# Kernel tuning notes

Hardware: AMD Instinct MI355X
Metric: run time of the kernel (lower is better)

The kernel has to match this reference:

```python
import jax, jax.numpy as jnp
import numpy as np
from jax import lax

B, L, C, P = 512, 6, 4, 45

def _conv(x, w, b, pad):
    y = lax.conv_general_dilated(x, w, (1, 1), [(pad, pad), (pad, pad)],
                                 dimension_numbers=('NCHW', 'OIHW', 'NCHW'))
    return y + b[None, :, None, None]

def _maxpool2(x):
    return lax.reduce_window(x, -jnp.inf, lax.max, (1, 1, 2, 2), (1, 1, 2, 2), 'VALID')

def _prelu(x, a):
    return jnp.where(x >= 0, x, a * x)

def setup_inputs() -> dict:
    key = jax.random.key(0)
    ks = jax.random.split(key, 16)
    s = 0.05
    inp = {
        'x': jax.random.normal(ks[0], (B, L, C, P, P), jnp.float32),
        'w0': jax.random.normal(ks[1], (32, C, 5, 5), jnp.float32) * s,
        'b0': jnp.zeros((32,), jnp.float32),
        'w1': jax.random.normal(ks[2], (32, 32, 5, 5), jnp.float32) * s,
        'b1': jnp.zeros((32,), jnp.float32),
        'w2': jax.random.normal(ks[3], (64, 32, 4, 4), jnp.float32) * s,
        'b2': jnp.zeros((64,), jnp.float32),
        'w3': jax.random.normal(ks[4], (64, 64, 3, 3), jnp.float32) * s,
        'b3': jnp.zeros((64,), jnp.float32),
        'a0': jnp.float32(0.25), 'a1': jnp.float32(0.25),
        'a2': jnp.float32(0.25), 'a3': jnp.float32(0.25),
        'fc1_w': jax.random.normal(ks[5], (L, 256, 128), jnp.float32) * s,
        'fc1_b': jnp.zeros((L, 128), jnp.float32),
        'a4': jnp.full((L, 1), 0.25, jnp.float32),
        'fc2_w': jax.random.normal(ks[6], (L, 128, 64), jnp.float32) * s,
        'fc2_b': jnp.zeros((L, 64), jnp.float32),
        'a5': jnp.full((L, 1), 0.25, jnp.float32),
        'fc3_w': jax.random.normal(ks[7], (L, 64, 4), jnp.float32) * s,
        'fc3_b': jnp.zeros((L, 4), jnp.float32),
    }
    return inp

def reference(x, w0, b0, w1, b1, w2, b2, w3, b3, a0, a1, a2, a3,
              fc1_w, fc1_b, a4, fc2_w, fc2_b, a5, fc3_w, fc3_b):
    b, l = x.shape[0], x.shape[1]
    # Conv tower shares weights across landmarks -> fold landmark into batch.
    h = x.reshape(b * l, x.shape[2], P, P)
    h = _maxpool2(_prelu(_conv(h, w0, b0, 1), a0))   # (BL,32,21,21)
    h = _maxpool2(_prelu(_conv(h, w1, b1, 1), a1))   # (BL,32,9,9)
    h = _maxpool2(_prelu(_conv(h, w2, b2, 1), a2))   # (BL,64,4,4)
    h = _prelu(_conv(h, w3, b3, 0), a3)              # (BL,64,2,2)
    h = h.reshape(b, l, 256)
    # Per-landmark FC heads as batched GEMMs.
    h = _prelu(jnp.einsum('bli,lio->blo', h, fc1_w) + fc1_b, a4)
    h = _prelu(jnp.einsum('bli,lio->blo', h, fc2_w) + fc2_b, a5)
    out = jnp.einsum('bli,lio->blo', h, fc3_w) + fc3_b   # (B,L,4)
    return out
```

## Files before the change

### kernel.cpp

```cpp
#include <hip/hip_runtime.h>
#include <stdint.h>

typedef _Float16 f16;
typedef _Float16 half8 __attribute__((ext_vector_type(8)));
typedef _Float16 half4 __attribute__((ext_vector_type(4)));
typedef float floatx16 __attribute__((ext_vector_type(16)));

#define NIMG 3072

#define WS_W0T   0
#define WS_W1T   10240
#define WS_W2T   61440
#define WS_W3T   126976
#define WS_FC1T  200704
#define WS_FC2T  593920
#define WS_FC3T  692224
#define WS_H3F   720896

#define Z16 {0.f,0.f,0.f,0.f,0.f,0.f,0.f,0.f,0.f,0.f,0.f,0.f,0.f,0.f,0.f,0.f}

__global__ __launch_bounds__(256) void k_prep(
    const float* __restrict__ w0, const float* __restrict__ w1, const float* __restrict__ w2,
    const float* __restrict__ w3, const float* __restrict__ fc1w, const float* __restrict__ fc2w,
    const float* __restrict__ fc3w,
    f16* __restrict__ w0t, f16* __restrict__ w1t, f16* __restrict__ w2t, f16* __restrict__ w3t,
    f16* __restrict__ fc1t, f16* __restrict__ fc2t, f16* __restrict__ fc3t)
{
  int stride = gridDim.x * blockDim.x;
  int g0 = blockIdx.x * blockDim.x + threadIdx.x;
  for (int i = g0; i < 5120; i += stride) {
    int j = i & 7, co = (i >> 3) & 31, hf = (i >> 8) & 1, ch = (i >> 9) & 1, ky = i >> 10;
    int k = ch * 16 + hf * 8 + j;
    f16 v = (f16)0.f;
    if (k < 20) { int kx = k >> 2, ci = k & 3; v = (f16)w0[((co * 4 + ci) * 5 + ky) * 5 + kx]; }
    w0t[i] = v;
  }
  for (int i = g0; i < 25600; i += stride) {
    int j = i & 7, co = (i >> 3) & 31, hf = (i >> 8) & 1, ch = (i >> 9) & 1, tap = i >> 10;
    int ci = ch * 16 + hf * 8 + j, ky = tap / 5, kx = tap % 5;
    w1t[i] = (f16)w1[((co * 32 + ci) * 5 + ky) * 5 + kx];
  }
  for (int i = g0; i < 32768; i += stride) {
    int j = i & 7, co = (i >> 3) & 31, hf = (i >> 8) & 1, ct = (i >> 9) & 1, ch = (i >> 10) & 1, tap = i >> 11;
    int ci = ch * 16 + hf * 8 + j, cog = ct * 32 + co, ky = tap >> 2, kx = tap & 3;
    w2t[i] = (f16)w2[((cog * 32 + ci) * 4 + ky) * 4 + kx];
  }
  for (int i = g0; i < 36864; i += stride) {
    int j = i & 7, col = (i >> 3) & 31, hf = (i >> 8) & 1, ct = (i >> 9) & 1, c = i >> 10;
    int k = c * 16 + hf * 8 + j, tap = k >> 6, ci = k & 63, co = ct * 32 + col;
    int ky = tap / 3, kx = tap % 3;
    w3t[i] = (f16)w3[((co * 64 + ci) * 3 + ky) * 3 + kx];
  }
  for (int i = g0; i < 196608; i += stride) {
    int j = i & 7, col = (i >> 3) & 31, hf = (i >> 8) & 1, nt = (i >> 9) & 3, c = (i >> 11) & 15, l = i >> 15;
    int k = c * 16 + hf * 8 + j, o = nt * 32 + col;
    fc1t[i] = (f16)fc1w[(l * 256 + k) * 128 + o];
  }
  for (int i = g0; i < 49152; i += stride) {
    int j = i & 7, col = (i >> 3) & 31, hf = (i >> 8) & 1, nt = (i >> 9) & 1, c = (i >> 10) & 7, l = i >> 13;
    int k = c * 16 + hf * 8 + j, o = nt * 32 + col;
    fc2t[i] = (f16)fc2w[(l * 128 + k) * 64 + o];
  }
  for (int i = g0; i < 12288; i += stride) {
    int j = i & 7, col = (i >> 3) & 31, hf = (i >> 8) & 1, c = (i >> 9) & 3, l = i >> 11;
    int k = c * 16 + hf * 8 + j;
    f16 v = (f16)0.f;
    if (col < 4) v = (f16)fc3w[(l * 64 + k) * 4 + col];
    fc3t[i] = v;
  }
}

__global__ __launch_bounds__(512) void k_conv012(
    const float* __restrict__ x,
    const f16* __restrict__ w0t, const float* __restrict__ b0, const float* __restrict__ a0p,
    const f16* __restrict__ w1t, const float* __restrict__ b1, const float* __restrict__ a1p,
    const f16* __restrict__ w2t, const float* __restrict__ b2, const float* __restrict__ a2p,
    f16* __restrict__ h3f)
{
  __shared__ __align__(16) uint32_t smem_u[16704];
  f16* sh   = (f16*)smem_u;
  f16* s_x  = sh;
  f16* s_h1 = sh + 10528;
  f16* s_h2 = sh;

  const int n = blockIdx.x, tid = threadIdx.x;
  const int wv = tid >> 6, l = tid & 63;
  const int hf = l >> 5, m = l & 31, dr = m >> 3, dc = m & 7, col = m;
  const float a0 = a0p[0], a1 = a1p[0];
  const float b0c = b0[col], b1c = b1[col];
  const half8* w0t8 = (const half8*)w0t;
  const half8* w1t8 = (const half8*)w1t;
  const half8* w2t8 = (const half8*)w2t;

  for (int i = tid; i < 16704; i += 512) smem_u[i] = 0u;
  __syncthreads();
  const float* xin = x + n * 8100;
  for (int i = tid; i < 8100; i += 512) {
    int ci = i / 2025, r = i % 2025;
    int y = r / 45, xx = r % 45;
    s_x[((y + 1) * 56 + (xx + 1)) * 4 + ci] = (f16)xin[i];
  }
  __syncthreads();

  half8 B0[5][2];
  #pragma unroll
  for (int ky = 0; ky < 5; ++ky)
    #pragma unroll
    for (int ch = 0; ch < 2; ++ch)
      B0[ky][ch] = w0t8[(ky * 2 + ch) * 64 + hf * 32 + col];

  const int r0lut0[11] = {0,4,8,12,16,20,24,28,32,36,38};
  for (int t = wv; t < 66; t += 8) {
    int r0 = r0lut0[t / 6], cb = (t % 6) * 8;
    int rowb = r0 + dr, colb = cb + dc;
    const f16* pA = s_x + (rowb * 56 + colb + 2 * hf) * 4;
    floatx16 acc = Z16;
    #pragma unroll
    for (int ky = 0; ky < 5; ++ky) {
      const f16* p = pA + ky * 224;
      half4 l0  = *(const half4*)(p);
      half4 h0  = *(const half4*)(p + 4);
      half4 l1  = *(const half4*)(p + 16);
      half4 h1v = *(const half4*)(p + 20);
      half8 a0v = __builtin_shufflevector(l0, h0, 0,1,2,3,4,5,6,7);
      half8 a1v = __builtin_shufflevector(l1, h1v, 0,1,2,3,4,5,6,7);
      acc = __builtin_amdgcn_mfma_f32_32x32x16_f16(a0v, B0[ky][0], acc, 0, 0, 0);
      acc = __builtin_amdgcn_mfma_f32_32x32x16_f16(a1v, B0[ky][1], acc, 0, 0, 0);
    }
    #pragma unroll
    for (int pp = 0; pp < 2; ++pp)
      #pragma unroll
      for (int c2 = 0; c2 < 2; ++c2) {
        float v = fmaxf(fmaxf(acc[8*pp + 2*c2], acc[8*pp + 2*c2 + 1]),
                        fmaxf(acc[8*pp + 4 + 2*c2], acc[8*pp + 4 + 2*c2 + 1]));
        v += b0c; v = (v >= 0.f) ? v : a0 * v;
        int pr = (r0 >> 1) + pp, pc = (cb >> 1) + 2 * hf + c2;
        if (pc < 21) s_h1[((pr + 1) * 26 + (pc + 1)) * 40 + col] = (f16)v;
      }
  }
  __syncthreads();

  for (int i = tid; i < 2880; i += 512) smem_u[i] = 0u;
  __syncthreads();

  const int r0lut1[5] = {0, 4, 8, 12, 14};
  const int cclut[3]  = {0, 8, 14};
  int t0 = wv * 2;
  int t1 = t0 + 1; if (t1 > 14) t1 = 14;
  int r0a = r0lut1[t0 / 3], cca = cclut[t0 % 3];
  int r0b = r0lut1[t1 / 3], ccb = cclut[t1 % 3];
  const f16* pAa = s_h1 + ((r0a + dr) * 26 + cca + dc) * 40 + hf * 8;
  const f16* pAb = s_h1 + ((r0b + dr) * 26 + ccb + dc) * 40 + hf * 8;
  floatx16 accA = Z16;
  floatx16 accB = Z16;
  for (int ky = 0; ky < 5; ++ky) {
    const half8* wb = w1t8 + ky * 640 + hf * 32 + col;
    const f16* qa = pAa + ky * 1040;
    const f16* qb = pAb + ky * 1040;
    #pragma unroll
    for (int kx = 0; kx < 5; ++kx) {
      #pragma unroll
      for (int ch = 0; ch < 2; ++ch) {
        half8 b  = wb[kx * 128 + ch * 64];
        half8 aA = *(const half8*)(qa + kx * 40 + ch * 16);
        half8 aB = *(const half8*)(qb + kx * 40 + ch * 16);
        accA = __builtin_amdgcn_mfma_f32_32x32x16_f16(aA, b, accA, 0, 0, 0);
        accB = __builtin_amdgcn_mfma_f32_32x32x16_f16(aB, b, accB, 0, 0, 0);
      }
    }
  }
  #pragma unroll
  for (int tt = 0; tt < 2; ++tt) {
    const floatx16 acc = tt ? accB : accA;
    int r0 = tt ? r0b : r0a, cc = tt ? ccb : cca;
    #pragma unroll
    for (int pp = 0; pp < 2; ++pp)
      #pragma unroll
      for (int c2 = 0; c2 < 2; ++c2) {
        float v = fmaxf(fmaxf(acc[8*pp + 2*c2], acc[8*pp + 2*c2 + 1]),
                        fmaxf(acc[8*pp + 4 + 2*c2], acc[8*pp + 4 + 2*c2 + 1]));
        v += b1c; v = (v >= 0.f) ? v : a1 * v;
        int pr = (r0 >> 1) + pp, pc = (cc >> 1) + 2 * hf + c2;
        if (pc < 9) s_h2[((pr + 1) * 12 + (pc + 1)) * 40 + col] = (f16)v;
      }
  }
  __syncthreads();

  if (wv < 2) {
    const int ct = wv;
    const float a2 = a2p[0];
    const float b2c = b2[ct * 32 + col];
    const f16* pA0 = s_h2 + (dr * 12 + dc) * 40 + hf * 8;
    const f16* pA4 = s_h2 + ((4 + dr) * 12 + dc) * 40 + hf * 8;
    floatx16 acc0 = Z16;
    floatx16 acc4 = Z16;
    for (int tap = 0; tap < 16; ++tap) {
      int ky = tap >> 2, kx = tap & 3;
      int aoff = (ky * 12 + kx) * 40;
      #pragma unroll
      for (int ch = 0; ch < 2; ++ch) {
        half8 b  = w2t8[tap * 256 + ch * 128 + ct * 64 + hf * 32 + col];
        half8 a0v = *(const half8*)(pA0 + aoff + ch * 16);
        half8 a4v = *(const half8*)(pA4 + aoff + ch * 16);
        acc0 = __builtin_amdgcn_mfma_f32_32x32x16_f16(a0v, b, acc0, 0, 0, 0);
        acc4 = __builtin_amdgcn_mfma_f32_32x32x16_f16(a4v, b, acc4, 0, 0, 0);
      }
    }
    f16* o = h3f + n * 1024;
    #pragma unroll
    for (int tt = 0; tt < 2; ++tt) {
      const floatx16 acc = tt ? acc4 : acc0;
      #pragma unroll
      for (int pp = 0; pp < 2; ++pp)
        #pragma unroll
        for (int c2 = 0; c2 < 2; ++c2) {
          float v = fmaxf(fmaxf(acc[8*pp + 2*c2], acc[8*pp + 2*c2 + 1]),
                          fmaxf(acc[8*pp + 4 + 2*c2], acc[8*pp + 4 + 2*c2 + 1]));
          v += b2c; v = (v >= 0.f) ? v : a2 * v;
          int pr = tt * 2 + pp, pc = 2 * hf + c2, co = ct * 32 + col;
          o[(pr * 4 + pc) * 64 + co] = (f16)v;
        }
    }
  }
}

__global__ __launch_bounds__(256) void k_tail(
    const f16* __restrict__ h3f,
    const f16* __restrict__ w3t, const float* __restrict__ b3, const float* __restrict__ a3p,
    const f16* __restrict__ fc1t, const float* __restrict__ fc1b, const float* __restrict__ a4,
    const f16* __restrict__ fc2t, const float* __restrict__ fc2b, const float* __restrict__ a5,
    const f16* __restrict__ fc3t, const float* __restrict__ fc3b,
    float* __restrict__ out)
{
  __shared__ __align__(16) f16 s_feat[32 * 264];
  __shared__ __align__(16) f16 s_g1[32 * 136];
  __shared__ __align__(16) f16 s_g2[32 * 72];

  const int lm = blockIdx.x % 6, t = blockIdx.x / 6;
  const int tid = threadIdx.x, wv = tid >> 6, lane = tid & 63;
  const int hf = lane >> 5, col = lane & 31;
  const half8* w3t8  = (const half8*)w3t;
  const half8* fc1t8 = (const half8*)fc1t;
  const half8* fc2t8 = (const half8*)fc2t;
  const half8* fc3t8 = (const half8*)fc3t;

  {
    const int mt = wv;
    const int i_img = mt * 8 + (col >> 2);
    const int pos = col & 3, oy = pos >> 1, ox = pos & 1;
    const int gimg = (t * 32 + i_img) * 6 + lm;
    const f16* Abase = h3f + gimg * 1024 + (oy * 4 + ox) * 64;
    floatx16 acc0 = Z16, acc1 = Z16;
    for (int c = 0; c < 36; ++c) {
      int tap = c >> 2;
      int ky = tap / 3, kx = tap % 3;
      half8 a = *(const half8*)(Abase + (ky * 4 + kx) * 64 + (c & 3) * 16 + hf * 8);
      half8 bb0 = w3t8[((c * 2 + 0) * 2 + hf) * 32 + col];
      half8 bb1 = w3t8[((c * 2 + 1) * 2 + hf) * 32 + col];
      acc0 = __builtin_amdgcn_mfma_f32_32x32x16_f16(a, bb0, acc0, 0, 0, 0);
      acc1 = __builtin_amdgcn_mfma_f32_32x32x16_f16(a, bb1, acc1, 0, 0, 0);
    }
    const float a3 = a3p[0];
    #pragma unroll
    for (int ct = 0; ct < 2; ++ct) {
      const floatx16 acc = ct ? acc1 : acc0;
      const int co = ct * 32 + col;
      const float bb = b3[co];
      #pragma unroll
      for (int q = 0; q < 4; ++q) {
        int ii = mt * 8 + 2 * q + hf;
        half4 w;
        #pragma unroll
        for (int z = 0; z < 4; ++z) {
          float v = acc[q * 4 + z] + bb;
          v = (v >= 0.f) ? v : a3 * v;
          w[z] = (f16)v;
        }
        *(half4*)(s_feat + ii * 264 + co * 4) = w;
      }
    }
  }
  __syncthreads();

  {
    floatx16 g = Z16;
    for (int c = 0; c < 16; ++c) {
      half8 a = *(const half8*)(s_feat + col * 264 + c * 16 + hf * 8);
      half8 b = fc1t8[(((lm * 16 + c) * 4 + wv) * 2 + hf) * 32 + col];
      g = __builtin_amdgcn_mfma_f32_32x32x16_f16(a, b, g, 0, 0, 0);
    }
    const float a4v = a4[lm];
    const float bb = fc1b[lm * 128 + wv * 32 + col];
    #pragma unroll
    for (int reg = 0; reg < 16; ++reg) {
      int r = (reg & 3) + 8 * (reg >> 2) + 4 * hf;
      float v = g[reg] + bb;
      v = (v >= 0.f) ? v : a4v * v;
      s_g1[r * 136 + wv * 32 + col] = (f16)v;
    }
  }
  __syncthreads();

  if (wv < 2) {
    floatx16 g = Z16;
    for (int c = 0; c < 8; ++c) {
      half8 a = *(const half8*)(s_g1 + col * 136 + c * 16 + hf * 8);
      half8 b = fc2t8[(((lm * 8 + c) * 2 + wv) * 2 + hf) * 32 + col];
      g = __builtin_amdgcn_mfma_f32_32x32x16_f16(a, b, g, 0, 0, 0);
    }
    const float a5v = a5[lm];
    const float bb = fc2b[lm * 64 + wv * 32 + col];
    #pragma unroll
    for (int reg = 0; reg < 16; ++reg) {
      int r = (reg & 3) + 8 * (reg >> 2) + 4 * hf;
      float v = g[reg] + bb;
      v = (v >= 0.f) ? v : a5v * v;
      s_g2[r * 72 + wv * 32 + col] = (f16)v;
    }
  }
  __syncthreads();

  if (wv == 0) {
    floatx16 g = Z16;
    for (int c = 0; c < 4; ++c) {
      half8 a = *(const half8*)(s_g2 + col * 72 + c * 16 + hf * 8);
      half8 b = fc3t8[((lm * 4 + c) * 2 + hf) * 32 + col];
      g = __builtin_amdgcn_mfma_f32_32x32x16_f16(a, b, g, 0, 0, 0);
    }
    if (col < 4) {
      const float bb = fc3b[lm * 4 + col];
      #pragma unroll
      for (int reg = 0; reg < 16; ++reg) {
        int r = (reg & 3) + 8 * (reg >> 2) + 4 * hf;
        out[((t * 32 + r) * 6 + lm) * 4 + col] = g[reg] + bb;
      }
    }
  }
}

extern "C" void kernel_launch(void* const* d_in, const int* in_sizes, int n_in,
                              void* d_out, int out_size, void* d_ws, size_t ws_size,
                              hipStream_t stream) {
  const float* x    = (const float*)d_in[0];
  const float* w0   = (const float*)d_in[1];
  const float* b0   = (const float*)d_in[2];
  const float* w1   = (const float*)d_in[3];
  const float* b1   = (const float*)d_in[4];
  const float* w2   = (const float*)d_in[5];
  const float* b2   = (const float*)d_in[6];
  const float* w3   = (const float*)d_in[7];
  const float* b3   = (const float*)d_in[8];
  const float* a0   = (const float*)d_in[9];
  const float* a1   = (const float*)d_in[10];
  const float* a2   = (const float*)d_in[11];
  const float* a3   = (const float*)d_in[12];
  const float* fc1w = (const float*)d_in[13];
  const float* fc1b = (const float*)d_in[14];
  const float* a4   = (const float*)d_in[15];
  const float* fc2w = (const float*)d_in[16];
  const float* fc2b = (const float*)d_in[17];
  const float* a5   = (const float*)d_in[18];
  const float* fc3w = (const float*)d_in[19];
  const float* fc3b = (const float*)d_in[20];
  float* out = (float*)d_out;

  char* ws = (char*)d_ws;
  f16* w0t  = (f16*)(ws + WS_W0T);
  f16* w1t  = (f16*)(ws + WS_W1T);
  f16* w2t  = (f16*)(ws + WS_W2T);
  f16* w3t  = (f16*)(ws + WS_W3T);
  f16* fc1t = (f16*)(ws + WS_FC1T);
  f16* fc2t = (f16*)(ws + WS_FC2T);
  f16* fc3t = (f16*)(ws + WS_FC3T);
  f16* h3f  = (f16*)(ws + WS_H3F);

  k_prep   <<<128, 256, 0, stream>>>(w0, w1, w2, w3, fc1w, fc2w, fc3w,
                                     w0t, w1t, w2t, w3t, fc1t, fc2t, fc3t);
  k_conv012<<<NIMG, 512, 0, stream>>>(x, w0t, b0, a0, w1t, b1, a1, w2t, b2, a2, h3f);
  k_tail   <<<96, 256, 0, stream>>>(h3f, w3t, b3, a3, fc1t, fc1b, a4,
                                    fc2t, fc2b, a5, fc3t, fc3b, out);
}
```

Before: 338.9 us.

## Fuse conv3 and per-landmark FC heads into the per-image conv kernel

Merges the tail kernel into the per-image conv kernel. Each block now computes conv3 and the three FC layers for its own image using scalar FMA dot products on shared-memory fp32 activations, in place of batched MFMA GEMMs over 32 images. This removes the h3f global round trip and one kernel launch. Each block now reads its landmark's FC weights, about 64K fp16 for fc1, so total weight traffic through L2 grows roughly 32x, and the conv2 stage is spread over four waves instead of two.

```diff
diff --git a/kernel.cpp b/kernel.cpp
--- a/kernel.cpp
+++ b/kernel.cpp
@@ -11,11 +11,10 @@
 #define WS_W0T   0
 #define WS_W1T   10240
 #define WS_W2T   61440
-#define WS_W3T   126976
-#define WS_FC1T  200704
-#define WS_FC2T  593920
-#define WS_FC3T  692224
-#define WS_H3F   720896
+#define WS_W3G   126976
+#define WS_FC1G  200704
+#define WS_FC2G  593920
+#define WS_FC3G  692224
 
 #define Z16 {0.f,0.f,0.f,0.f,0.f,0.f,0.f,0.f,0.f,0.f,0.f,0.f,0.f,0.f,0.f,0.f}
 
@@ -23,8 +22,8 @@
     const float* __restrict__ w0, const float* __restrict__ w1, const float* __restrict__ w2,
     const float* __restrict__ w3, const float* __restrict__ fc1w, const float* __restrict__ fc2w,
     const float* __restrict__ fc3w,
-    f16* __restrict__ w0t, f16* __restrict__ w1t, f16* __restrict__ w2t, f16* __restrict__ w3t,
-    f16* __restrict__ fc1t, f16* __restrict__ fc2t, f16* __restrict__ fc3t)
+    f16* __restrict__ w0t, f16* __restrict__ w1t, f16* __restrict__ w2t,
+    f16* __restrict__ w3g, f16* __restrict__ fc1g, f16* __restrict__ fc2g, f16* __restrict__ fc3g)
 {
   int stride = gridDim.x * blockDim.x;
   int g0 = blockIdx.x * blockDim.x + threadIdx.x;
@@ -46,44 +45,47 @@
     w2t[i] = (f16)w2[((cog * 32 + ci) * 4 + ky) * 4 + kx];
   }
   for (int i = g0; i < 36864; i += stride) {
-    int j = i & 7, col = (i >> 3) & 31, hf = (i >> 8) & 1, ct = (i >> 9) & 1, c = i >> 10;
-    int k = c * 16 + hf * 8 + j, tap = k >> 6, ci = k & 63, co = ct * 32 + col;
-    int ky = tap / 3, kx = tap % 3;
-    w3t[i] = (f16)w3[((co * 64 + ci) * 3 + ky) * 3 + kx];
+    int co = i / 576, k = i % 576;
+    int tap = k >> 6, ci = k & 63, ky = tap / 3, kx = tap % 3;
+    w3g[i] = (f16)w3[((co * 64 + ci) * 3 + ky) * 3 + kx];
   }
   for (int i = g0; i < 196608; i += stride) {
-    int j = i & 7, col = (i >> 3) & 31, hf = (i >> 8) & 1, nt = (i >> 9) & 3, c = (i >> 11) & 15, l = i >> 15;
-    int k = c * 16 + hf * 8 + j, o = nt * 32 + col;
-    fc1t[i] = (f16)fc1w[(l * 256 + k) * 128 + o];
+    int l = i >> 15, o = (i >> 8) & 127, k = i & 255;
+    fc1g[i] = (f16)fc1w[(l * 256 + k) * 128 + o];
   }
   for (int i = g0; i < 49152; i += stride) {
-    int j = i & 7, col = (i >> 3) & 31, hf = (i >> 8) & 1, nt = (i >> 9) & 1, c = (i >> 10) & 7, l = i >> 13;
-    int k = c * 16 + hf * 8 + j, o = nt * 32 + col;
-    fc2t[i] = (f16)fc2w[(l * 128 + k) * 64 + o];
-  }
-  for (int i = g0; i < 12288; i += stride) {
-    int j = i & 7, col = (i >> 3) & 31, hf = (i >> 8) & 1, c = (i >> 9) & 3, l = i >> 11;
-    int k = c * 16 + hf * 8 + j;
-    f16 v = (f16)0.f;
-    if (col < 4) v = (f16)fc3w[(l * 64 + k) * 4 + col];
-    fc3t[i] = v;
+    int l = i >> 13, o = (i >> 7) & 63, k = i & 127;
+    fc2g[i] = (f16)fc2w[(l * 128 + k) * 64 + o];
+  }
+  for (int i = g0; i < 1536; i += stride) {
+    int l = i >> 8, o = (i >> 6) & 3, k = i & 63;
+    fc3g[i] = (f16)fc3w[(l * 64 + k) * 4 + o];
   }
 }
 
-__global__ __launch_bounds__(512) void k_conv012(
+__global__ __launch_bounds__(512) void k_all(
     const float* __restrict__ x,
     const f16* __restrict__ w0t, const float* __restrict__ b0, const float* __restrict__ a0p,
     const f16* __restrict__ w1t, const float* __restrict__ b1, const float* __restrict__ a1p,
     const f16* __restrict__ w2t, const float* __restrict__ b2, const float* __restrict__ a2p,
-    f16* __restrict__ h3f)
+    const f16* __restrict__ w3g, const float* __restrict__ b3, const float* __restrict__ a3p,
+    const f16* __restrict__ fc1g, const float* __restrict__ fc1b, const float* __restrict__ a4,
+    const f16* __restrict__ fc2g, const float* __restrict__ fc2b, const float* __restrict__ a5,
+    const f16* __restrict__ fc3g, const float* __restrict__ fc3b,
+    float* __restrict__ out)
 {
   __shared__ __align__(16) uint32_t smem_u[16704];
   f16* sh   = (f16*)smem_u;
   f16* s_x  = sh;
   f16* s_h1 = sh + 10528;
   f16* s_h2 = sh;
+  float* s_h3 = (float*)(sh + 5760);
+  float* s_h4 = (float*)(sh + 7808);
+  float* s_g1 = (float*)(sh + 8320);
+  float* s_g2 = (float*)(sh + 8576);
 
   const int n = blockIdx.x, tid = threadIdx.x;
+  const int lm = n % 6;
   const int wv = tid >> 6, l = tid & 63;
   const int hf = l >> 5, m = l & 31, dr = m >> 3, dc = m & 7, col = m;
   const float a0 = a0p[0], a1 = a1p[0];
@@ -186,155 +188,142 @@
   }
   __syncthreads();
 
-  if (wv < 2) {
-    const int ct = wv;
+  if (wv < 4) {
+    const int mt = wv >> 1, ct = wv & 1;
     const float a2 = a2p[0];
     const float b2c = b2[ct * 32 + col];
-    const f16* pA0 = s_h2 + (dr * 12 + dc) * 40 + hf * 8;
-    const f16* pA4 = s_h2 + ((4 + dr) * 12 + dc) * 40 + hf * 8;
-    floatx16 acc0 = Z16;
-    floatx16 acc4 = Z16;
+    const f16* pA = s_h2 + ((mt * 4 + dr) * 12 + dc) * 40 + hf * 8;
+    floatx16 acc = Z16;
     for (int tap = 0; tap < 16; ++tap) {
       int ky = tap >> 2, kx = tap & 3;
       int aoff = (ky * 12 + kx) * 40;
       #pragma unroll
       for (int ch = 0; ch < 2; ++ch) {
         half8 b  = w2t8[tap * 256 + ch * 128 + ct * 64 + hf * 32 + col];
-        half8 a0v = *(const half8*)(pA0 + aoff + ch * 16);
-        half8 a4v = *(const half8*)(pA4 + aoff + ch * 16);
-        acc0 = __builtin_amdgcn_mfma_f32_32x32x16_f16(a0v, b, acc0, 0, 0, 0);
-        acc4 = __builtin_amdgcn_mfma_f32_32x32x16_f16(a4v, b, acc4, 0, 0, 0);
-      }
-    }
-    f16* o = h3f + n * 1024;
-    #pragma unroll
-    for (int tt = 0; tt < 2; ++tt) {
-      const floatx16 acc = tt ? acc4 : acc0;
-      #pragma unroll
-      for (int pp = 0; pp < 2; ++pp)
+        half8 av = *(const half8*)(pA + aoff + ch * 16);
+        acc = __builtin_amdgcn_mfma_f32_32x32x16_f16(av, b, acc, 0, 0, 0);
+      }
+    }
+    #pragma unroll
+    for (int pp = 0; pp < 2; ++pp)
+      #pragma unroll
+      for (int c2 = 0; c2 < 2; ++c2) {
+        float v = fmaxf(fmaxf(acc[8*pp + 2*c2], acc[8*pp + 2*c2 + 1]),
+                        fmaxf(acc[8*pp + 4 + 2*c2], acc[8*pp + 4 + 2*c2 + 1]));
+        v += b2c; v = (v >= 0.f) ? v : a2 * v;
+        int pr = mt * 2 + pp, pc = 2 * hf + c2, co = ct * 32 + col;
+        s_h3[(pr * 4 + pc) * 64 + co] = v;
+      }
+  }
+  __syncthreads();
+
+  {
+    const int out_id = tid >> 1, kh = tid & 1;
+    const int co3 = out_id >> 2, pos3 = out_id & 3;
+    const int oy = pos3 >> 1, ox = pos3 & 1;
+    float acc = 0.f;
+    const f16* wr = w3g + co3 * 576 + kh * 32;
+    #pragma unroll
+    for (int ky = 0; ky < 3; ++ky)
+      #pragma unroll
+      for (int kx = 0; kx < 3; ++kx) {
+        const int ipos = (oy + ky) * 4 + (ox + kx);
+        const float* hp = s_h3 + ipos * 64 + kh * 32;
+        const half8* w8p = (const half8*)(wr + (ky * 3 + kx) * 64);
         #pragma unroll
-        for (int c2 = 0; c2 < 2; ++c2) {
-          float v = fmaxf(fmaxf(acc[8*pp + 2*c2], acc[8*pp + 2*c2 + 1]),
-                          fmaxf(acc[8*pp + 4 + 2*c2], acc[8*pp + 4 + 2*c2 + 1]));
-          v += b2c; v = (v >= 0.f) ? v : a2 * v;
-          int pr = tt * 2 + pp, pc = 2 * hf + c2, co = ct * 32 + col;
-          o[(pr * 4 + pc) * 64 + co] = (f16)v;
+        for (int q = 0; q < 4; ++q) {
+          half8 w8 = w8p[q];
+          float4 h0v = *(const float4*)(hp + q * 8);
+          float4 h1v = *(const float4*)(hp + q * 8 + 4);
+          acc = fmaf((float)w8[0], h0v.x, acc);
+          acc = fmaf((float)w8[1], h0v.y, acc);
+          acc = fmaf((float)w8[2], h0v.z, acc);
+          acc = fmaf((float)w8[3], h0v.w, acc);
+          acc = fmaf((float)w8[4], h1v.x, acc);
+          acc = fmaf((float)w8[5], h1v.y, acc);
+          acc = fmaf((float)w8[6], h1v.z, acc);
+          acc = fmaf((float)w8[7], h1v.w, acc);
         }
-    }
-  }
-}
-
-__global__ __launch_bounds__(256) void k_tail(
-    const f16* __restrict__ h3f,
-    const f16* __restrict__ w3t, const float* __restrict__ b3, const float* __restrict__ a3p,
-    const f16* __restrict__ fc1t, const float* __restrict__ fc1b, const float* __restrict__ a4,
-    const f16* __restrict__ fc2t, const float* __restrict__ fc2b, const float* __restrict__ a5,
-    const f16* __restrict__ fc3t, const float* __restrict__ fc3b,
-    float* __restrict__ out)
-{
-  __shared__ __align__(16) f16 s_feat[32 * 264];
-  __shared__ __align__(16) f16 s_g1[32 * 136];
-  __shared__ __align__(16) f16 s_g2[32 * 72];
-
-  const int lm = blockIdx.x % 6, t = blockIdx.x / 6;
-  const int tid = threadIdx.x, wv = tid >> 6, lane = tid & 63;
-  const int hf = lane >> 5, col = lane & 31;
-  const half8* w3t8  = (const half8*)w3t;
-  const half8* fc1t8 = (const half8*)fc1t;
-  const half8* fc2t8 = (const half8*)fc2t;
-  const half8* fc3t8 = (const half8*)fc3t;
+      }
+    acc += __shfl_xor(acc, 1, 64);
+    if (kh == 0) {
+      float v = acc + b3[co3];
+      v = (v >= 0.f) ? v : a3p[0] * v;
+      s_h4[out_id] = v;
+    }
+  }
+  __syncthreads();
 
   {
-    const int mt = wv;
-    const int i_img = mt * 8 + (col >> 2);
-    const int pos = col & 3, oy = pos >> 1, ox = pos & 1;
-    const int gimg = (t * 32 + i_img) * 6 + lm;
-    const f16* Abase = h3f + gimg * 1024 + (oy * 4 + ox) * 64;
-    floatx16 acc0 = Z16, acc1 = Z16;
-    for (int c = 0; c < 36; ++c) {
-      int tap = c >> 2;
-      int ky = tap / 3, kx = tap % 3;
-      half8 a = *(const half8*)(Abase + (ky * 4 + kx) * 64 + (c & 3) * 16 + hf * 8);
-      half8 bb0 = w3t8[((c * 2 + 0) * 2 + hf) * 32 + col];
-      half8 bb1 = w3t8[((c * 2 + 1) * 2 + hf) * 32 + col];
-      acc0 = __builtin_amdgcn_mfma_f32_32x32x16_f16(a, bb0, acc0, 0, 0, 0);
-      acc1 = __builtin_amdgcn_mfma_f32_32x32x16_f16(a, bb1, acc1, 0, 0, 0);
-    }
-    const float a3 = a3p[0];
-    #pragma unroll
-    for (int ct = 0; ct < 2; ++ct) {
-      const floatx16 acc = ct ? acc1 : acc0;
-      const int co = ct * 32 + col;
-      const float bb = b3[co];
-      #pragma unroll
-      for (int q = 0; q < 4; ++q) {
-        int ii = mt * 8 + 2 * q + hf;
-        half4 w;
-        #pragma unroll
-        for (int z = 0; z < 4; ++z) {
-          float v = acc[q * 4 + z] + bb;
-          v = (v >= 0.f) ? v : a3 * v;
-          w[z] = (f16)v;
-        }
-        *(half4*)(s_feat + ii * 264 + co * 4) = w;
-      }
+    const int o = tid >> 2, kq = tid & 3;
+    float acc = 0.f;
+    const half8* w8p = (const half8*)(fc1g + ((lm * 128 + o) << 8) + kq * 64);
+    const float* hp = s_h4 + kq * 64;
+    #pragma unroll
+    for (int q = 0; q < 8; ++q) {
+      half8 w8 = w8p[q];
+      float4 h0v = *(const float4*)(hp + q * 8);
+      float4 h1v = *(const float4*)(hp + q * 8 + 4);
+      acc = fmaf((float)w8[0], h0v.x, acc);
+      acc = fmaf((float)w8[1], h0v.y, acc);
+      acc = fmaf((float)w8[2], h0v.z, acc);
+      acc = fmaf((float)w8[3], h0v.w, acc);
+      acc = fmaf((float)w8[4], h1v.x, acc);
+      acc = fmaf((float)w8[5], h1v.y, acc);
+      acc = fmaf((float)w8[6], h1v.z, acc);
+      acc = fmaf((float)w8[7], h1v.w, acc);
+    }
+    acc += __shfl_xor(acc, 1, 64);
+    acc += __shfl_xor(acc, 2, 64);
+    if (kq == 0) {
+      float v = acc + fc1b[lm * 128 + o];
+      v = (v >= 0.f) ? v : a4[lm] * v;
+      s_g1[o] = v;
     }
   }
   __syncthreads();
 
   {
-    floatx16 g = Z16;
-    for (int c = 0; c < 16; ++c) {
-      half8 a = *(const half8*)(s_feat + col * 264 + c * 16 + hf * 8);
-      half8 b = fc1t8[(((lm * 16 + c) * 4 + wv) * 2 + hf) * 32 + col];
-      g = __builtin_amdgcn_mfma_f32_32x32x16_f16(a, b, g, 0, 0, 0);
-    }
-    const float a4v = a4[lm];
-    const float bb = fc1b[lm * 128 + wv * 32 + col];
-    #pragma unroll
-    for (int reg = 0; reg < 16; ++reg) {
-      int r = (reg & 3) + 8 * (reg >> 2) + 4 * hf;
-      float v = g[reg] + bb;
-      v = (v >= 0.f) ? v : a4v * v;
-      s_g1[r * 136 + wv * 32 + col] = (f16)v;
-    }
-  }
-  __syncthreads();
-
-  if (wv < 2) {
-    floatx16 g = Z16;
-    for (int c = 0; c < 8; ++c) {
-      half8 a = *(const half8*)(s_g1 + col * 136 + c * 16 + hf * 8);
-      half8 b = fc2t8[(((lm * 8 + c) * 2 + wv) * 2 + hf) * 32 + col];
-      g = __builtin_amdgcn_mfma_f32_32x32x16_f16(a, b, g, 0, 0, 0);
-    }
-    const float a5v = a5[lm];
-    const float bb = fc2b[lm * 64 + wv * 32 + col];
-    #pragma unroll
-    for (int reg = 0; reg < 16; ++reg) {
-      int r = (reg & 3) + 8 * (reg >> 2) + 4 * hf;
-      float v = g[reg] + bb;
-      v = (v >= 0.f) ? v : a5v * v;
-      s_g2[r * 72 + wv * 32 + col] = (f16)v;
-    }
-  }
-  __syncthreads();
-
-  if (wv == 0) {
-    floatx16 g = Z16;
-    for (int c = 0; c < 4; ++c) {
-      half8 a = *(const half8*)(s_g2 + col * 72 + c * 16 + hf * 8);
-      half8 b = fc3t8[((lm * 4 + c) * 2 + hf) * 32 + col];
-      g = __builtin_amdgcn_mfma_f32_32x32x16_f16(a, b, g, 0, 0, 0);
-    }
-    if (col < 4) {
-      const float bb = fc3b[lm * 4 + col];
-      #pragma unroll
-      for (int reg = 0; reg < 16; ++reg) {
-        int r = (reg & 3) + 8 * (reg >> 2) + 4 * hf;
-        out[((t * 32 + r) * 6 + lm) * 4 + col] = g[reg] + bb;
-      }
-    }
+    const int o = tid >> 3, kq = tid & 7;
+    float acc = 0.f;
+    const half8* w8p = (const half8*)(fc2g + ((lm * 64 + o) << 7) + kq * 16);
+    const float* hp = s_g1 + kq * 16;
+    #pragma unroll
+    for (int q = 0; q < 2; ++q) {
+      half8 w8 = w8p[q];
+      float4 h0v = *(const float4*)(hp + q * 8);
+      float4 h1v = *(const float4*)(hp + q * 8 + 4);
+      acc = fmaf((float)w8[0], h0v.x, acc);
+      acc = fmaf((float)w8[1], h0v.y, acc);
+      acc = fmaf((float)w8[2], h0v.z, acc);
+      acc = fmaf((float)w8[3], h0v.w, acc);
+      acc = fmaf((float)w8[4], h1v.x, acc);
+      acc = fmaf((float)w8[5], h1v.y, acc);
+      acc = fmaf((float)w8[6], h1v.z, acc);
+      acc = fmaf((float)w8[7], h1v.w, acc);
+    }
+    acc += __shfl_xor(acc, 1, 64);
+    acc += __shfl_xor(acc, 2, 64);
+    acc += __shfl_xor(acc, 4, 64);
+    if (kq == 0) {
+      float v = acc + fc2b[lm * 64 + o];
+      v = (v >= 0.f) ? v : a5[lm] * v;
+      s_g2[o] = v;
+    }
+  }
+  __syncthreads();
+
+  if (tid < 64) {
+    const int o = tid >> 4, kq = tid & 15;
+    half4 w4 = *(const half4*)(fc3g + lm * 256 + o * 64 + kq * 4);
+    float4 hv = *(const float4*)(s_g2 + kq * 4);
+    float acc = (float)w4[0] * hv.x + (float)w4[1] * hv.y +
+                (float)w4[2] * hv.z + (float)w4[3] * hv.w;
+    acc += __shfl_xor(acc, 1, 64);
+    acc += __shfl_xor(acc, 2, 64);
+    acc += __shfl_xor(acc, 4, 64);
+    acc += __shfl_xor(acc, 8, 64);
+    if (kq == 0) out[n * 4 + o] = acc + fc3b[lm * 4 + o];
   }
 }
 
@@ -368,15 +357,15 @@
   f16* w0t  = (f16*)(ws + WS_W0T);
   f16* w1t  = (f16*)(ws + WS_W1T);
   f16* w2t  = (f16*)(ws + WS_W2T);
-  f16* w3t  = (f16*)(ws + WS_W3T);
-  f16* fc1t = (f16*)(ws + WS_FC1T);
-  f16* fc2t = (f16*)(ws + WS_FC2T);
-  f16* fc3t = (f16*)(ws + WS_FC3T);
-  f16* h3f  = (f16*)(ws + WS_H3F);
-
-  k_prep   <<<128, 256, 0, stream>>>(w0, w1, w2, w3, fc1w, fc2w, fc3w,
-                                     w0t, w1t, w2t, w3t, fc1t, fc2t, fc3t);
-  k_conv012<<<NIMG, 512, 0, stream>>>(x, w0t, b0, a0, w1t, b1, a1, w2t, b2, a2, h3f);
-  k_tail   <<<96, 256, 0, stream>>>(h3f, w3t, b3, a3, fc1t, fc1b, a4,
-                                    fc2t, fc2b, a5, fc3t, fc3b, out);
+  f16* w3g  = (f16*)(ws + WS_W3G);
+  f16* fc1g = (f16*)(ws + WS_FC1G);
+  f16* fc2g = (f16*)(ws + WS_FC2G);
+  f16* fc3g = (f16*)(ws + WS_FC3G);
+
+  k_prep<<<128, 256, 0, stream>>>(w0, w1, w2, w3, fc1w, fc2w, fc3w,
+                                  w0t, w1t, w2t, w3g, fc1g, fc2g, fc3g);
+  k_all <<<NIMG, 512, 0, stream>>>(x,
+                                   w0t, b0, a0, w1t, b1, a1, w2t, b2, a2,
+                                   w3g, b3, a3, fc1g, fc1b, a4,
+                                   fc2g, fc2b, a5, fc3g, fc3b, out);
 }
```

Result: slower. 388.9 us (+14.8%).

## Streamline conv012 indexing, separate h2 buffer, and split conv2 across four waves

Applied to the files above, without the earlier changes.

The shared buffer grows so s_h2 gets its own region, which removes the second zero-fill pass and its barrier. Zeroing now uses 16-byte stores. The input staging loop updates y/x/channel indices incrementally instead of using divisions, and the tile lookup tables are replaced by arithmetic. Conv2 is spread over four waves with one accumulator each instead of two waves with two. Several loops are marked unroll 1 to cut register pressure. The extra LDS per block may lower occupancy.

```diff
diff --git a/kernel.cpp b/kernel.cpp
--- a/kernel.cpp
+++ b/kernel.cpp
@@ -77,11 +77,11 @@
     const f16* __restrict__ w2t, const float* __restrict__ b2, const float* __restrict__ a2p,
     f16* __restrict__ h3f)
 {
-  __shared__ __align__(16) uint32_t smem_u[16704];
+  __shared__ __align__(16) uint32_t smem_u[19584];
   f16* sh   = (f16*)smem_u;
   f16* s_x  = sh;
   f16* s_h1 = sh + 10528;
-  f16* s_h2 = sh;
+  f16* s_h2 = sh + 33408;
 
   const int n = blockIdx.x, tid = threadIdx.x;
   const int wv = tid >> 6, l = tid & 63;
@@ -92,13 +92,25 @@
   const half8* w1t8 = (const half8*)w1t;
   const half8* w2t8 = (const half8*)w2t;
 
-  for (int i = tid; i < 16704; i += 512) smem_u[i] = 0u;
-  __syncthreads();
-  const float* xin = x + n * 8100;
-  for (int i = tid; i < 8100; i += 512) {
-    int ci = i / 2025, r = i % 2025;
-    int y = r / 45, xx = r % 45;
-    s_x[((y + 1) * 56 + (xx + 1)) * 4 + ci] = (f16)xin[i];
+  {
+    uint4 zz = {0u, 0u, 0u, 0u};
+    uint4* z = (uint4*)smem_u;
+    for (int i = tid; i < 4896; i += 512) z[i] = zz;
+  }
+  __syncthreads();
+
+  {
+    const float* xin = x + n * 8100;
+    int idx = tid;
+    int y = tid / 45, xx = tid - y * 45, ci = 0;
+    #pragma unroll 1
+    for (int it = 0; it < 16; ++it) {
+      if (idx < 8100) s_x[((y + 1) * 56 + (xx + 1)) * 4 + ci] = (f16)xin[idx];
+      idx += 512;
+      xx += 17; y += 11;
+      if (xx >= 45) { xx -= 45; ++y; }
+      if (y >= 45) { y -= 45; ++ci; }
+    }
   }
   __syncthreads();
 
@@ -109,118 +121,116 @@
     for (int ch = 0; ch < 2; ++ch)
       B0[ky][ch] = w0t8[(ky * 2 + ch) * 64 + hf * 32 + col];
 
-  const int r0lut0[11] = {0,4,8,12,16,20,24,28,32,36,38};
-  for (int t = wv; t < 66; t += 8) {
-    int r0 = r0lut0[t / 6], cb = (t % 6) * 8;
-    int rowb = r0 + dr, colb = cb + dc;
-    const f16* pA = s_x + (rowb * 56 + colb + 2 * hf) * 4;
-    floatx16 acc = Z16;
-    #pragma unroll
-    for (int ky = 0; ky < 5; ++ky) {
-      const f16* p = pA + ky * 224;
-      half4 l0  = *(const half4*)(p);
-      half4 h0  = *(const half4*)(p + 4);
-      half4 l1  = *(const half4*)(p + 16);
-      half4 h1v = *(const half4*)(p + 20);
-      half8 a0v = __builtin_shufflevector(l0, h0, 0,1,2,3,4,5,6,7);
-      half8 a1v = __builtin_shufflevector(l1, h1v, 0,1,2,3,4,5,6,7);
-      acc = __builtin_amdgcn_mfma_f32_32x32x16_f16(a0v, B0[ky][0], acc, 0, 0, 0);
-      acc = __builtin_amdgcn_mfma_f32_32x32x16_f16(a1v, B0[ky][1], acc, 0, 0, 0);
-    }
-    #pragma unroll
-    for (int pp = 0; pp < 2; ++pp)
-      #pragma unroll
-      for (int c2 = 0; c2 < 2; ++c2) {
-        float v = fmaxf(fmaxf(acc[8*pp + 2*c2], acc[8*pp + 2*c2 + 1]),
-                        fmaxf(acc[8*pp + 4 + 2*c2], acc[8*pp + 4 + 2*c2 + 1]));
-        v += b0c; v = (v >= 0.f) ? v : a0 * v;
-        int pr = (r0 >> 1) + pp, pc = (cb >> 1) + 2 * hf + c2;
-        if (pc < 21) s_h1[((pr + 1) * 26 + (pc + 1)) * 40 + col] = (f16)v;
-      }
-  }
-  __syncthreads();
-
-  for (int i = tid; i < 2880; i += 512) smem_u[i] = 0u;
-  __syncthreads();
-
-  const int r0lut1[5] = {0, 4, 8, 12, 14};
-  const int cclut[3]  = {0, 8, 14};
-  int t0 = wv * 2;
-  int t1 = t0 + 1; if (t1 > 14) t1 = 14;
-  int r0a = r0lut1[t0 / 3], cca = cclut[t0 % 3];
-  int r0b = r0lut1[t1 / 3], ccb = cclut[t1 % 3];
-  const f16* pAa = s_h1 + ((r0a + dr) * 26 + cca + dc) * 40 + hf * 8;
-  const f16* pAb = s_h1 + ((r0b + dr) * 26 + ccb + dc) * 40 + hf * 8;
-  floatx16 accA = Z16;
-  floatx16 accB = Z16;
-  for (int ky = 0; ky < 5; ++ky) {
-    const half8* wb = w1t8 + ky * 640 + hf * 32 + col;
-    const f16* qa = pAa + ky * 1040;
-    const f16* qb = pAb + ky * 1040;
-    #pragma unroll
-    for (int kx = 0; kx < 5; ++kx) {
-      #pragma unroll
-      for (int ch = 0; ch < 2; ++ch) {
-        half8 b  = wb[kx * 128 + ch * 64];
-        half8 aA = *(const half8*)(qa + kx * 40 + ch * 16);
-        half8 aB = *(const half8*)(qb + kx * 40 + ch * 16);
-        accA = __builtin_amdgcn_mfma_f32_32x32x16_f16(aA, b, accA, 0, 0, 0);
-        accB = __builtin_amdgcn_mfma_f32_32x32x16_f16(aB, b, accB, 0, 0, 0);
-      }
-    }
-  }
-  #pragma unroll
-  for (int tt = 0; tt < 2; ++tt) {
-    const floatx16 acc = tt ? accB : accA;
-    int r0 = tt ? r0b : r0a, cc = tt ? ccb : cca;
-    #pragma unroll
-    for (int pp = 0; pp < 2; ++pp)
-      #pragma unroll
-      for (int c2 = 0; c2 < 2; ++c2) {
-        float v = fmaxf(fmaxf(acc[8*pp + 2*c2], acc[8*pp + 2*c2 + 1]),
-                        fmaxf(acc[8*pp + 4 + 2*c2], acc[8*pp + 4 + 2*c2 + 1]));
-        v += b1c; v = (v >= 0.f) ? v : a1 * v;
-        int pr = (r0 >> 1) + pp, pc = (cc >> 1) + 2 * hf + c2;
-        if (pc < 9) s_h2[((pr + 1) * 12 + (pc + 1)) * 40 + col] = (f16)v;
-      }
-  }
-  __syncthreads();
-
-  if (wv < 2) {
-    const int ct = wv;
-    const float a2 = a2p[0];
-    const float b2c = b2[ct * 32 + col];
-    const f16* pA0 = s_h2 + (dr * 12 + dc) * 40 + hf * 8;
-    const f16* pA4 = s_h2 + ((4 + dr) * 12 + dc) * 40 + hf * 8;
-    floatx16 acc0 = Z16;
-    floatx16 acc4 = Z16;
-    for (int tap = 0; tap < 16; ++tap) {
-      int ky = tap >> 2, kx = tap & 3;
-      int aoff = (ky * 12 + kx) * 40;
-      #pragma unroll
-      for (int ch = 0; ch < 2; ++ch) {
-        half8 b  = w2t8[tap * 256 + ch * 128 + ct * 64 + hf * 32 + col];
-        half8 a0v = *(const half8*)(pA0 + aoff + ch * 16);
-        half8 a4v = *(const half8*)(pA4 + aoff + ch * 16);
-        acc0 = __builtin_amdgcn_mfma_f32_32x32x16_f16(a0v, b, acc0, 0, 0, 0);
-        acc4 = __builtin_amdgcn_mfma_f32_32x32x16_f16(a4v, b, acc4, 0, 0, 0);
-      }
-    }
-    f16* o = h3f + n * 1024;
-    #pragma unroll
-    for (int tt = 0; tt < 2; ++tt) {
-      const floatx16 acc = tt ? acc4 : acc0;
+  {
+    int tr = 0, tc = wv;
+    if (tc >= 6) { tc -= 6; tr = 1; }
+    #pragma unroll 1
+    for (int t = wv; t < 66; t += 8) {
+      int r0 = min(tr * 4, 38), cb = tc * 8;
+      int rowb = r0 + dr, colb = cb + dc;
+      const f16* pA = s_x + (rowb * 56 + colb + 2 * hf) * 4;
+      floatx16 acc = Z16;
+      #pragma unroll
+      for (int ky = 0; ky < 5; ++ky) {
+        const f16* p = pA + ky * 224;
+        half4 l0  = *(const half4*)(p);
+        half4 h0  = *(const half4*)(p + 4);
+        half4 l1  = *(const half4*)(p + 16);
+        half4 h1v = *(const half4*)(p + 20);
+        half8 a0v = __builtin_shufflevector(l0, h0, 0,1,2,3,4,5,6,7);
+        half8 a1v = __builtin_shufflevector(l1, h1v, 0,1,2,3,4,5,6,7);
+        acc = __builtin_amdgcn_mfma_f32_32x32x16_f16(a0v, B0[ky][0], acc, 0, 0, 0);
+        acc = __builtin_amdgcn_mfma_f32_32x32x16_f16(a1v, B0[ky][1], acc, 0, 0, 0);
+      }
       #pragma unroll
       for (int pp = 0; pp < 2; ++pp)
         #pragma unroll
         for (int c2 = 0; c2 < 2; ++c2) {
           float v = fmaxf(fmaxf(acc[8*pp + 2*c2], acc[8*pp + 2*c2 + 1]),
                           fmaxf(acc[8*pp + 4 + 2*c2], acc[8*pp + 4 + 2*c2 + 1]));
-          v += b2c; v = (v >= 0.f) ? v : a2 * v;
-          int pr = tt * 2 + pp, pc = 2 * hf + c2, co = ct * 32 + col;
-          o[(pr * 4 + pc) * 64 + co] = (f16)v;
+          v += b0c; v = (v >= 0.f) ? v : a0 * v;
+          int pr = (r0 >> 1) + pp, pc = (cb >> 1) + 2 * hf + c2;
+          if (pc < 21) s_h1[((pr + 1) * 26 + (pc + 1)) * 40 + col] = (f16)v;
         }
-    }
+      tc += 2; tr += 1;
+      if (tc >= 6) { tc -= 6; ++tr; }
+    }
+  }
+  __syncthreads();
+
+  {
+    int t0 = wv * 2;
+    int t1 = t0 + 1; if (t1 > 14) t1 = 14;
+    int q0 = (t0 * 11) >> 5, q1 = (t1 * 11) >> 5;
+    int r0a = min(q0 * 4, 14), cca = min((t0 - 3 * q0) * 8, 14);
+    int r0b = min(q1 * 4, 14), ccb = min((t1 - 3 * q1) * 8, 14);
+    const f16* pAa = s_h1 + ((r0a + dr) * 26 + cca + dc) * 40 + hf * 8;
+    const f16* pAb = s_h1 + ((r0b + dr) * 26 + ccb + dc) * 40 + hf * 8;
+    floatx16 accA = Z16;
+    floatx16 accB = Z16;
+    #pragma unroll 1
+    for (int ky = 0; ky < 5; ++ky) {
+      const half8* wb = w1t8 + ky * 640 + hf * 32 + col;
+      const f16* qa = pAa + ky * 1040;
+      const f16* qb = pAb + ky * 1040;
+      #pragma unroll
+      for (int kx = 0; kx < 5; ++kx) {
+        #pragma unroll
+        for (int ch = 0; ch < 2; ++ch) {
+          half8 b  = wb[kx * 128 + ch * 64];
+          half8 aA = *(const half8*)(qa + kx * 40 + ch * 16);
+          half8 aB = *(const half8*)(qb + kx * 40 + ch * 16);
+          accA = __builtin_amdgcn_mfma_f32_32x32x16_f16(aA, b, accA, 0, 0, 0);
+          accB = __builtin_amdgcn_mfma_f32_32x32x16_f16(aB, b, accB, 0, 0, 0);
+        }
+      }
+    }
+    #pragma unroll
+    for (int tt = 0; tt < 2; ++tt) {
+      const floatx16 acc = tt ? accB : accA;
+      int r0 = tt ? r0b : r0a, cc = tt ? ccb : cca;
+      #pragma unroll
+      for (int pp = 0; pp < 2; ++pp)
+        #pragma unroll
+        for (int c2 = 0; c2 < 2; ++c2) {
+          float v = fmaxf(fmaxf(acc[8*pp + 2*c2], acc[8*pp + 2*c2 + 1]),
+                          fmaxf(acc[8*pp + 4 + 2*c2], acc[8*pp + 4 + 2*c2 + 1]));
+          v += b1c; v = (v >= 0.f) ? v : a1 * v;
+          int pr = (r0 >> 1) + pp, pc = (cc >> 1) + 2 * hf + c2;
+          if (pc < 9) s_h2[((pr + 1) * 12 + (pc + 1)) * 40 + col] = (f16)v;
+        }
+    }
+  }
+  __syncthreads();
+
+  if (wv < 4) {
+    const int mt = wv >> 1, ct = wv & 1;
+    const float a2 = a2p[0];
+    const float b2c = b2[ct * 32 + col];
+    const f16* pA = s_h2 + ((mt * 4 + dr) * 12 + dc) * 40 + hf * 8;
+    floatx16 acc = Z16;
+    #pragma unroll 1
+    for (int tap = 0; tap < 16; ++tap) {
+      int ky = tap >> 2, kx = tap & 3;
+      int aoff = (ky * 12 + kx) * 40;
+      #pragma unroll
+      for (int ch = 0; ch < 2; ++ch) {
+        half8 b  = w2t8[tap * 256 + ch * 128 + ct * 64 + hf * 32 + col];
+        half8 av = *(const half8*)(pA + aoff + ch * 16);
+        acc = __builtin_amdgcn_mfma_f32_32x32x16_f16(av, b, acc, 0, 0, 0);
+      }
+    }
+    f16* o = h3f + n * 1024;
+    #pragma unroll
+    for (int pp = 0; pp < 2; ++pp)
+      #pragma unroll
+      for (int c2 = 0; c2 < 2; ++c2) {
+        float v = fmaxf(fmaxf(acc[8*pp + 2*c2], acc[8*pp + 2*c2 + 1]),
+                        fmaxf(acc[8*pp + 4 + 2*c2], acc[8*pp + 4 + 2*c2 + 1]));
+        v += b2c; v = (v >= 0.f) ? v : a2 * v;
+        int pr = mt * 2 + pp, pc = 2 * hf + c2, co = ct * 32 + col;
+        o[(pr * 4 + pc) * 64 + co] = (f16)v;
+      }
   }
 }
 
```

Result: slower. 363.1 us (+7.2%).
